# Kernel tuning notes

Hardware: AMD Instinct MI355X
Metric: run time of the kernel (lower is better)

The kernel has to match this reference:

```python
import jax, jax.numpy as jnp
import numpy as np

ALPHA = 0.01  # LeakyReLU negative slope
NEG_INF = -1e12

def setup_inputs() -> dict:
    key = jax.random.key(0)
    k1, k2, k3, k4 = jax.random.split(key, 4)
    B, N, F_in, F_out = 8, 2048, 256, 128
    inp = jax.random.normal(k1, (B, N, F_in), dtype=jnp.float32)
    adj = jax.random.randint(k2, (B, N, N), 0, 2, dtype=jnp.int32)
    # xavier_uniform with gain=1.414
    limW = 1.414 * np.sqrt(6.0 / (F_in + F_out))
    W = jax.random.uniform(k3, (F_in, F_out), minval=-limW, maxval=limW, dtype=jnp.float32)
    lima = 1.414 * np.sqrt(6.0 / (2 * F_out + 1))
    a = jax.random.uniform(k4, (2 * F_out, 1), minval=-lima, maxval=lima, dtype=jnp.float32)
    return {"inp": inp, "adj": adj, "W": W, "a": a}

def reference(inp, adj, W, a):
    # h: [B, N, F_out]
    h = jnp.matmul(inp, W)
    F_out = W.shape[1]
    # Algebraic split of the attention vector: a = [a1; a2], so
    # e[b,i,j] = leakyrelu(h_i . a1 + h_j . a2)  -- avoids the O(N^2*2F) a_input.
    a1 = a[:F_out, 0]   # [F_out]
    a2 = a[F_out:, 0]   # [F_out]
    s1 = jnp.einsum('bnf,f->bn', h, a1)  # [B, N] source term
    s2 = jnp.einsum('bnf,f->bn', h, a2)  # [B, N] target term
    e = s1[:, :, None] + s2[:, None, :]  # [B, N, N]
    e = jnp.where(e > 0, e, ALPHA * e)   # leaky relu
    scores = jnp.where(adj > 0, e, NEG_INF)
    attention = jax.nn.softmax(scores, axis=2)  # [B, N, N]
    h_prime = jnp.matmul(attention, h)          # [B, N, F_out]
    return jax.nn.relu(h_prime)  # concat=True branch
```

## Files before the change

kernel.cpp:

```cpp
#include <hip/hip_runtime.h>
#include <hip/hip_bf16.h>

#define N_    2048
#define FIN   256
#define FOUT  128
#define ALPHA 0.01f

typedef short bf16x8 __attribute__((ext_vector_type(8)));
typedef float f32x4  __attribute__((ext_vector_type(4)));

static __device__ __forceinline__ unsigned short f2bf(float x) {
    __hip_bfloat16 h = __float2bfloat16(x);
    return *reinterpret_cast<unsigned short*>(&h);
}

__global__ __launch_bounds__(256) void k_lin(
    const float* __restrict__ inp, const float* __restrict__ W,
    const float* __restrict__ av, __hip_bfloat16* __restrict__ hT,
    float* __restrict__ s1, float* __restrict__ s2)
{
    __shared__ float in_lds[32 * FIN];
    int g = blockIdx.x;
    int b = g & 7;
    int tile = g >> 3;
    int i0 = tile << 5;
    int t = threadIdx.x;

    const float4* src = reinterpret_cast<const float4*>(inp + ((size_t)(b * N_ + i0)) * FIN);
    float4* dst = reinterpret_cast<float4*>(in_lds);
#pragma unroll
    for (int c = 0; c < 8; ++c) dst[t + 256 * c] = src[t + 256 * c];
    __syncthreads();

    int fq = t & 31;
    int rg = t >> 5;
    float acc[4][4];
#pragma unroll
    for (int r = 0; r < 4; ++r)
#pragma unroll
        for (int j = 0; j < 4; ++j) acc[r][j] = 0.f;

    const float4* W4 = reinterpret_cast<const float4*>(W);
    for (int k = 0; k < FIN; k += 4) {
        float4 inr[4];
#pragma unroll
        for (int r = 0; r < 4; ++r)
            inr[r] = *reinterpret_cast<const float4*>(&in_lds[(rg * 4 + r) * FIN + k]);
#pragma unroll
        for (int kk = 0; kk < 4; ++kk) {
            float4 w4 = W4[(k + kk) * 32 + fq];
#pragma unroll
            for (int r = 0; r < 4; ++r) {
                float iv = (&inr[r].x)[kk];
                acc[r][0] = fmaf(iv, w4.x, acc[r][0]);
                acc[r][1] = fmaf(iv, w4.y, acc[r][1]);
                acc[r][2] = fmaf(iv, w4.z, acc[r][2]);
                acc[r][3] = fmaf(iv, w4.w, acc[r][3]);
            }
        }
    }

    float a1v[4], a2v[4];
#pragma unroll
    for (int j = 0; j < 4; ++j) {
        a1v[j] = av[fq * 4 + j];
        a2v[j] = av[FOUT + fq * 4 + j];
    }
#pragma unroll
    for (int r = 0; r < 4; ++r) {
        float p1 = acc[r][0] * a1v[0] + acc[r][1] * a1v[1] + acc[r][2] * a1v[2] + acc[r][3] * a1v[3];
        float p2 = acc[r][0] * a2v[0] + acc[r][1] * a2v[1] + acc[r][2] * a2v[2] + acc[r][3] * a2v[3];
#pragma unroll
        for (int off = 1; off < 32; off <<= 1) {
            p1 += __shfl_xor(p1, off);
            p2 += __shfl_xor(p2, off);
        }
        if (fq == 0) {
            int row = i0 + rg * 4 + r;
            s1[b * N_ + row] = p1;
            s2[b * N_ + row] = p2;
        }
    }

    __syncthreads();
    unsigned short* hb = reinterpret_cast<unsigned short*>(in_lds);
#pragma unroll
    for (int j = 0; j < 4; ++j)
#pragma unroll
        for (int r = 0; r < 4; ++r)
            hb[(fq * 4 + j) * 33 + rg * 4 + r] = f2bf(acc[r][j]);
    __syncthreads();
    {
        int f = t >> 1;
        int c0 = (t & 1) * 16;
        unsigned short tmp[16];
#pragma unroll
        for (int c = 0; c < 16; ++c) tmp[c] = hb[f * 33 + c0 + c];
        int4* dst4 = reinterpret_cast<int4*>(&hT[((size_t)(b * FOUT + f)) * N_ + i0 + c0]);
        dst4[0] = reinterpret_cast<const int4*>(tmp)[0];
        dst4[1] = reinterpret_cast<const int4*>(tmp)[1];
    }
}

__global__ __launch_bounds__(256) void k_s2max(const float* __restrict__ s2,
                                               float* __restrict__ s2max)
{
    __shared__ float red[4];
    int b = blockIdx.x, t = threadIdx.x;
    const float4* p = reinterpret_cast<const float4*>(s2 + b * N_);
    float4 v0 = p[t], v1 = p[t + 256];
    float m = fmaxf(fmaxf(fmaxf(v0.x, v0.y), fmaxf(v0.z, v0.w)),
                    fmaxf(fmaxf(v1.x, v1.y), fmaxf(v1.z, v1.w)));
#pragma unroll
    for (int off = 1; off < 64; off <<= 1) m = fmaxf(m, __shfl_xor(m, off));
    if ((t & 63) == 0) red[t >> 6] = m;
    __syncthreads();
    if (t == 0) s2max[b] = fmaxf(fmaxf(red[0], red[1]), fmaxf(red[2], red[3]));
}

__global__ __launch_bounds__(256, 4) void k_attn(
    const int* __restrict__ adj, const __hip_bfloat16* __restrict__ hT,
    const float* __restrict__ s1g, const float* __restrict__ s2g,
    const float* __restrict__ s2maxg, float* __restrict__ out)
{
    __shared__ float accb[4][16][128];
    __shared__ float l_s[4][16];

    int g = blockIdx.x;
    int b = g & 7;
    int tile = g >> 3;
    int i0 = tile << 4;
    int t = threadIdx.x;
    int w = t >> 6;
    int l = t & 63;
    int r = l & 15;
    int lg = l >> 4;
    int jc = w * 512;

    const float s1r = s1g[b * N_ + i0 + r];
    float eb = s1r + s2maxg[b];
    const float m_row = fmaxf(eb, ALPHA * eb);

    const int4* adjp = reinterpret_cast<const int4*>(
        adj + ((size_t)(b * N_ + i0 + r)) * N_ + jc + lg * 8);
    const float4* s2p = reinterpret_cast<const float4*>(s2g + b * N_ + jc + lg * 8);
    const bf16x8* hv = reinterpret_cast<const bf16x8*>(hT);
    size_t h0 = (((size_t)(b * FOUT + r)) * N_ + jc + lg * 8) >> 3;
    const size_t FRAG = (size_t)16 * N_ / 8;

    float l_run = 0.0f;
    f32x4 acc[8];
#pragma unroll
    for (int q = 0; q < 8; ++q) acc[q] = (f32x4){0.f, 0.f, 0.f, 0.f};

    int4 aj0 = adjp[0], aj1 = adjp[1];
    float4 s2a = s2p[0], s2b = s2p[1];

    for (int step = 0; step < 16; ++step) {
        int4 c0 = aj0, c1 = aj1;
        float4 ca = s2a, cb = s2b;
        if (step < 15) {
            aj0 = adjp[(step + 1) * 8];
            aj1 = adjp[(step + 1) * 8 + 1];
            s2a = s2p[(step + 1) * 8];
            s2b = s2p[(step + 1) * 8 + 1];
        }
        float sv[8] = {ca.x, ca.y, ca.z, ca.w, cb.x, cb.y, cb.z, cb.w};
        int am[8] = {c0.x, c0.y, c0.z, c0.w, c1.x, c1.y, c1.z, c1.w};

        bf16x8 af;
        float ps = 0.f;
#pragma unroll
        for (int e = 0; e < 8; ++e) {
            float v = s1r + sv[e];
            v = fmaxf(v, ALPHA * v);
            float p = (am[e] > 0) ? __expf(v - m_row) : 0.f;
            ps += p;
            af[e] = (short)f2bf(p);
        }
        l_run += ps;

#pragma unroll
        for (int q = 0; q < 8; ++q) {
            bf16x8 bfr = hv[h0 + (size_t)q * FRAG + step * 4];
            acc[q] = __builtin_amdgcn_mfma_f32_16x16x32_bf16(af, bfr, acc[q], 0, 0, 0);
        }
    }

    l_run += __shfl_xor(l_run, 16);
    l_run += __shfl_xor(l_run, 32);
    if (l < 16) l_s[w][l] = l_run;

#pragma unroll
    for (int q = 0; q < 8; ++q)
#pragma unroll
        for (int rr = 0; rr < 4; ++rr)
            accb[w][lg * 4 + rr][q * 16 + r] = acc[q][rr];
    __syncthreads();

    int f = t & 127;
    int rh = t >> 7;
#pragma unroll
    for (int rr = 0; rr < 8; ++rr) {
        int row = rh * 8 + rr;
        float L = l_s[0][row] + l_s[1][row] + l_s[2][row] + l_s[3][row];
        float v = accb[0][row][f] + accb[1][row][f] + accb[2][row][f] + accb[3][row][f];
        v = v / L;
        out[((size_t)(b * N_ + i0 + row)) * FOUT + f] = fmaxf(v, 0.f);
    }
}

extern "C" void kernel_launch(void* const* d_in, const int* in_sizes, int n_in,
                              void* d_out, int out_size, void* d_ws, size_t ws_size,
                              hipStream_t stream) {
    (void)in_sizes; (void)n_in; (void)out_size; (void)ws_size;
    const float* inp = (const float*)d_in[0];
    const int*   adj = (const int*)d_in[1];
    const float* W   = (const float*)d_in[2];
    const float* a   = (const float*)d_in[3];
    float* out = (float*)d_out;

    char* ws = (char*)d_ws;
    __hip_bfloat16* hT = (__hip_bfloat16*)ws;
    float* s1 = (float*)(ws + (size_t)8 * FOUT * N_ * 2);
    float* s2 = s1 + 8 * N_;
    float* s2max = s2 + 8 * N_;

    k_lin<<<512, 256, 0, stream>>>(inp, W, a, hT, s1, s2);
    k_s2max<<<8, 256, 0, stream>>>(s2, s2max);
    k_attn<<<1024, 256, 0, stream>>>(adj, hT, s1, s2, s2max, out);
}
```

Baseline: 286.6 us.

## Double-buffer hT fragments and adj loads, stage s2 in LDS in attention kernel

Restructures the k_attn main loop into a two-deep software pipeline. The adjacency rows are prefetched two steps ahead and the hT MFMA B-fragments one step ahead, in ping-pong register buffers. The s2 vector is now staged once per block into shared memory instead of being read from global memory every step. The occupancy hint in launch_bounds is dropped, because the larger register footprint (16 bf16x8 fragments) would otherwise force spills. In exchange, the kernel may run fewer waves per SIMD and uses 8 KB more LDS.

```diff
diff --git a/kernel.cpp b/kernel.cpp
--- a/kernel.cpp
+++ b/kernel.cpp
@@ -118,11 +118,12 @@
     if (t == 0) s2max[b] = fmaxf(fmaxf(red[0], red[1]), fmaxf(red[2], red[3]));
 }
 
-__global__ __launch_bounds__(256, 4) void k_attn(
+__global__ __launch_bounds__(256) void k_attn(
     const int* __restrict__ adj, const __hip_bfloat16* __restrict__ hT,
     const float* __restrict__ s1g, const float* __restrict__ s2g,
     const float* __restrict__ s2maxg, float* __restrict__ out)
 {
+    __shared__ float s2_lds[N_];
     __shared__ float accb[4][16][128];
     __shared__ float l_s[4][16];
 
@@ -137,37 +138,41 @@
     int lg = l >> 4;
     int jc = w * 512;
 
+    {
+        const float4* s2g4 = reinterpret_cast<const float4*>(s2g + b * N_);
+        reinterpret_cast<float4*>(s2_lds)[t] = s2g4[t];
+        reinterpret_cast<float4*>(s2_lds)[t + 256] = s2g4[t + 256];
+    }
+
     const float s1r = s1g[b * N_ + i0 + r];
     float eb = s1r + s2maxg[b];
     const float m_row = fmaxf(eb, ALPHA * eb);
 
     const int4* adjp = reinterpret_cast<const int4*>(
         adj + ((size_t)(b * N_ + i0 + r)) * N_ + jc + lg * 8);
-    const float4* s2p = reinterpret_cast<const float4*>(s2g + b * N_ + jc + lg * 8);
-    const bf16x8* hv = reinterpret_cast<const bf16x8*>(hT);
-    size_t h0 = (((size_t)(b * FOUT + r)) * N_ + jc + lg * 8) >> 3;
-    const size_t FRAG = (size_t)16 * N_ / 8;
+    const bf16x8* hvp = reinterpret_cast<const bf16x8*>(hT)
+        + ((((size_t)(b * FOUT + r)) * N_ + jc + lg * 8) >> 3);
+
+    __syncthreads();
 
     float l_run = 0.0f;
     f32x4 acc[8];
 #pragma unroll
     for (int q = 0; q < 8; ++q) acc[q] = (f32x4){0.f, 0.f, 0.f, 0.f};
 
-    int4 aj0 = adjp[0], aj1 = adjp[1];
-    float4 s2a = s2p[0], s2b = s2p[1];
-
-    for (int step = 0; step < 16; ++step) {
-        int4 c0 = aj0, c1 = aj1;
-        float4 ca = s2a, cb = s2b;
-        if (step < 15) {
-            aj0 = adjp[(step + 1) * 8];
-            aj1 = adjp[(step + 1) * 8 + 1];
-            s2a = s2p[(step + 1) * 8];
-            s2b = s2p[(step + 1) * 8 + 1];
-        }
+    int4 ajA0, ajA1, ajB0, ajB1;
+    bf16x8 hA[8], hB[8];
+
+    auto pf_hv = [&](bf16x8 (&hd)[8], int S) {
+#pragma unroll
+        for (int q = 0; q < 8; ++q) hd[q] = hvp[q * 4096 + S * 4];
+    };
+    auto compute_step = [&](int S, int4 c0, int4 c1, const bf16x8 (&hc)[8]) {
+        const float* s2b = &s2_lds[jc + S * 32 + lg * 8];
+        float4 ca = *reinterpret_cast<const float4*>(s2b);
+        float4 cb = *reinterpret_cast<const float4*>(s2b + 4);
         float sv[8] = {ca.x, ca.y, ca.z, ca.w, cb.x, cb.y, cb.z, cb.w};
         int am[8] = {c0.x, c0.y, c0.z, c0.w, c1.x, c1.y, c1.z, c1.w};
-
         bf16x8 af;
         float ps = 0.f;
 #pragma unroll
@@ -179,12 +184,38 @@
             af[e] = (short)f2bf(p);
         }
         l_run += ps;
-
-#pragma unroll
-        for (int q = 0; q < 8; ++q) {
-            bf16x8 bfr = hv[h0 + (size_t)q * FRAG + step * 4];
-            acc[q] = __builtin_amdgcn_mfma_f32_16x16x32_bf16(af, bfr, acc[q], 0, 0, 0);
-        }
+#pragma unroll
+        for (int q = 0; q < 8; ++q)
+            acc[q] = __builtin_amdgcn_mfma_f32_16x16x32_bf16(af, hc[q], acc[q], 0, 0, 0);
+    };
+
+    ajA0 = adjp[0];  ajA1 = adjp[1];
+    ajB0 = adjp[8];  ajB1 = adjp[9];
+    pf_hv(hA, 0);
+
+#pragma unroll 1
+    for (int it = 0; it < 7; ++it) {
+        const int sE = 2 * it;
+        {
+            int4 c0 = ajA0, c1 = ajA1;
+            ajA0 = adjp[(sE + 2) * 8];
+            ajA1 = adjp[(sE + 2) * 8 + 1];
+            pf_hv(hB, sE + 1);
+            compute_step(sE, c0, c1, hA);
+        }
+        {
+            int4 c0 = ajB0, c1 = ajB1;
+            ajB0 = adjp[(sE + 3) * 8];
+            ajB1 = adjp[(sE + 3) * 8 + 1];
+            pf_hv(hA, sE + 2);
+            compute_step(sE + 1, c0, c1, hB);
+        }
+    }
+    {
+        int4 c0 = ajA0, c1 = ajA1;
+        pf_hv(hB, 15);
+        compute_step(14, c0, c1, hA);
+        compute_step(15, ajB0, ajB1, hB);
     }
 
     l_run += __shfl_xor(l_run, 16);
```

Result: no change. 288.2 us (+0.5%).
